# Performance work log

Measured on AMD Instinct MI355X. Metric: run time of the kernel, lower is better.

## Reference

```python
import jax, jax.numpy as jnp
import numpy as np

BS, SEQ, DIM, HEADS = 2, 2048, 1024, 16
HEAD_DIM = DIM // HEADS
NEG = -1e9


def setup_inputs() -> dict:
    key = jax.random.key(0)
    ks = jax.random.split(key, 5)
    s = 1.0 / np.sqrt(DIM)
    return {
        "x": jax.random.normal(ks[0], (BS, SEQ, DIM), jnp.float32),
        "padding_mask": jnp.ones((BS, SEQ), jnp.int32),
        "causal_mask": jnp.tril(jnp.ones((SEQ, SEQ), jnp.int32)),
        "Wq": jax.random.normal(ks[1], (DIM, DIM), jnp.float32) * s,
        "bq": jnp.zeros((DIM,), jnp.float32),
        "Wk": jax.random.normal(ks[2], (DIM, DIM), jnp.float32) * s,
        "bk": jnp.zeros((DIM,), jnp.float32),
        "Wv": jax.random.normal(ks[3], (DIM, DIM), jnp.float32) * s,
        "bv": jnp.zeros((DIM,), jnp.float32),
        "Wo": jax.random.normal(ks[4], (DIM, DIM), jnp.float32) * s,
        "bo": jnp.zeros((DIM,), jnp.float32),
    }


def reference(x, padding_mask, causal_mask, Wq, bq, Wk, bk, Wv, bv, Wo, bo):
    bs, seq, dim = x.shape
    # QKV projections -> [b, h, s, d]
    def proj(W, b):
        return (x @ W.T + b).reshape(bs, seq, HEADS, HEAD_DIM).transpose(0, 2, 1, 3)
    q, k, v = proj(Wq, bq), proj(Wk, bk), proj(Wv, bv)
    scores = jnp.einsum("bhqd,bhkd->bhqk", q, k) / np.sqrt(HEAD_DIM).astype(np.float32)
    scores = jnp.where(padding_mask[:, None, None, :] == 0, NEG, scores)
    scores = jnp.where(causal_mask[None, None, :, :] == 0, NEG, scores)
    attn = jax.nn.softmax(scores, axis=-1)
    out = jnp.einsum("bhqk,bhkd->bhqd", attn, v)
    out = out.transpose(0, 2, 1, 3).reshape(bs, seq, dim)
    return out @ Wo.T + bo
```

## Files before the change

### kernel.cpp

```cpp
#include <hip/hip_runtime.h>
#include <hip/hip_bf16.h>
#include <stdint.h>

#define SEQ 2048
#define DIM 1024
#define HEADS 16
#define HD 64
#define NEGV (-1e9f)
#define SCALE2 0.18033688011112042f
#define THR2 11.541560327111707f

typedef __attribute__((ext_vector_type(8))) short short8;
typedef __attribute__((ext_vector_type(4))) float f32x4;

__device__ __forceinline__ unsigned short f2bf(float f) {
  __hip_bfloat16 h = __float2bfloat16(f);
  union { __hip_bfloat16 h; unsigned short u; } cv;
  cv.h = h;
  return cv.u;
}

__device__ __forceinline__ void async16(const void* g, void* l) {
  __builtin_amdgcn_global_load_lds(
      (const __attribute__((address_space(1))) unsigned int*)g,
      (__attribute__((address_space(3))) unsigned int*)l, 16, 0, 0);
}

__global__ void cast_all_k(const float* __restrict__ x,
                           const float* __restrict__ w0, const float* __restrict__ w1,
                           const float* __restrict__ w2, const float* __restrict__ w3,
                           unsigned short* __restrict__ xo,
                           unsigned short* __restrict__ o0, unsigned short* __restrict__ o1,
                           unsigned short* __restrict__ o2, unsigned short* __restrict__ o3,
                           int nx4, int nw4) {
  const int seg = blockIdx.y;
  const float* in = (seg == 0) ? x : (seg == 1) ? w0 : (seg == 2) ? w1
                   : (seg == 3) ? w2 : w3;
  unsigned short* out = (seg == 0) ? xo : (seg == 1) ? o0 : (seg == 2) ? o1
                       : (seg == 3) ? o2 : o3;
  const int n4 = (seg == 0) ? nx4 : nw4;
  int stride = gridDim.x * blockDim.x;
  for (int i = blockIdx.x * blockDim.x + threadIdx.x; i < n4; i += stride) {
    float4 v = ((const float4*)in)[i];
    ushort4 o;
    o.x = f2bf(v.x); o.y = f2bf(v.y); o.z = f2bf(v.z); o.w = f2bf(v.w);
    ((ushort4*)out)[i] = o;
  }
}

__device__ __forceinline__ void stage_ab(const unsigned short* __restrict__ A,
                                         const unsigned short* __restrict__ B,
                                         int K, int bm0, int bn0, int k0,
                                         unsigned short* As, unsigned short* Bs,
                                         int tid) {
#pragma unroll
  for (int i = 0; i < 2; ++i) {
    int e   = (i * 256 + tid) * 8;
    int row = e >> 5;
    int kk  = e & 31;
    async16(A + (size_t)(bm0 + row) * K + (size_t)(k0 + kk), As + e);
    async16(B + (size_t)(bn0 + row) * K + (size_t)(k0 + kk), Bs + e);
  }
}

__device__ __forceinline__ void gemm_core(const unsigned short* __restrict__ A,
                                          const unsigned short* __restrict__ B,
                                          int K, int bm0, int bn0,
                                          unsigned short (*As)[128 * 32],
                                          unsigned short (*Bs)[128 * 32],
                                          f32x4 acc[4][4]) {
  const int tid  = threadIdx.x;
  const int lane = tid & 63;
  const int w    = tid >> 6;
  const int wr   = w >> 1, wc = w & 1;
  const int lrow = lane & 15, lkg = lane >> 4;

  stage_ab(A, B, K, bm0, bn0, 0, As[0], Bs[0], tid);
  __syncthreads();

  for (int k0 = 0; k0 < K; k0 += 32) {
    const int cur = (k0 >> 5) & 1;
    if (k0 + 32 < K)
      stage_ab(A, B, K, bm0, bn0, k0 + 32, As[cur ^ 1], Bs[cur ^ 1], tid);

    short8 af[4], bf[4];
#pragma unroll
    for (int i = 0; i < 4; ++i) {
      af[i] = *(const short8*)(As[cur] + (wr * 64 + i * 16 + lrow) * 32 + lkg * 8);
      bf[i] = *(const short8*)(Bs[cur] + (wc * 64 + i * 16 + lrow) * 32 + lkg * 8);
    }
#pragma unroll
    for (int i = 0; i < 4; ++i)
#pragma unroll
      for (int j = 0; j < 4; ++j)
        acc[i][j] = __builtin_amdgcn_mfma_f32_16x16x32_bf16(af[i], bf[j], acc[i][j], 0, 0, 0);

    __syncthreads();
  }
}

__global__ __launch_bounds__(256)
void qkv_gemm_k(const unsigned short* __restrict__ xb,
                const unsigned short* __restrict__ wqb,
                const unsigned short* __restrict__ wkb,
                const unsigned short* __restrict__ wvb,
                const float* __restrict__ bq, const float* __restrict__ bk,
                const float* __restrict__ bv,
                unsigned short* __restrict__ Qb, unsigned short* __restrict__ Kb,
                unsigned short* __restrict__ Vtb) {
  __shared__ __align__(16) unsigned short As[2][128 * 32];
  __shared__ __align__(16) unsigned short Bs[2][128 * 32];
  const int z = blockIdx.z;
  const unsigned short* B = (z == 0) ? wqb : (z == 1) ? wkb : wvb;
  const float* bias       = (z == 0) ? bq  : (z == 1) ? bk  : bv;
  const int bm0 = blockIdx.y * 128, bn0 = blockIdx.x * 128;

  f32x4 acc[4][4] = {};
  gemm_core(xb, B, DIM, bm0, bn0, As, Bs, acc);

  const int lane = threadIdx.x & 63;
  const int w = threadIdx.x >> 6, wr = w >> 1, wc = w & 1;
  unsigned short* out01 = (z == 0) ? Qb : Kb;
  const float oscale = (z == 0) ? SCALE2 : 1.0f;
#pragma unroll
  for (int i = 0; i < 4; ++i)
#pragma unroll
    for (int j = 0; j < 4; ++j)
#pragma unroll
      for (int r = 0; r < 4; ++r) {
        int mg = bm0 + wr * 64 + i * 16 + (lane >> 4) * 4 + r;
        int ng = bn0 + wc * 64 + j * 16 + (lane & 15);
        float v = (acc[i][j][r] + bias[ng]) * oscale;
        int bb = mg >> 11, s = mg & 2047, h = ng >> 6, d = ng & 63;
        int bh = bb * HEADS + h;
        if (z < 2)
          out01[((size_t)bh * SEQ + s) * HD + d] = f2bf(v);
        else
          Vtb[((size_t)bh * HD + d) * SEQ + s] = f2bf(v);
      }
}

__global__ __launch_bounds__(256)
void out_gemm_k(const unsigned short* __restrict__ Ob,
                const unsigned short* __restrict__ wob,
                const float* __restrict__ bo, float* __restrict__ out) {
  __shared__ __align__(16) unsigned short As[2][128 * 32];
  __shared__ __align__(16) unsigned short Bs[2][128 * 32];
  const int bm0 = blockIdx.y * 128, bn0 = blockIdx.x * 128;

  f32x4 acc[4][4] = {};
  gemm_core(Ob, wob, DIM, bm0, bn0, As, Bs, acc);

  const int lane = threadIdx.x & 63;
  const int w = threadIdx.x >> 6, wr = w >> 1, wc = w & 1;
#pragma unroll
  for (int i = 0; i < 4; ++i)
#pragma unroll
    for (int j = 0; j < 4; ++j)
#pragma unroll
      for (int r = 0; r < 4; ++r) {
        int mg = bm0 + wr * 64 + i * 16 + (lane >> 4) * 4 + r;
        int ng = bn0 + wc * 64 + j * 16 + (lane & 15);
        out[(size_t)mg * DIM + ng] = acc[i][j][r] + bo[ng];
      }
}

__device__ __forceinline__ void stage_kv64(const unsigned short* __restrict__ kbase,
                                           const unsigned short* __restrict__ vbase,
                                           int k0, unsigned short* KsB,
                                           unsigned short* VsB, int tid) {
#pragma unroll
  for (int j = 0; j < 2; ++j) {
    const int c    = j * 256 + tid;
    const int row  = c >> 3;
    const int colb = (c & 7) << 4;
    const int srcb = colb ^ ((row & 7) << 4);
    async16(kbase + (size_t)(k0 + row) * HD + (srcb >> 1), KsB + c * 8);
  }
#pragma unroll
  for (int j = 0; j < 2; ++j) {
    const int c    = j * 256 + tid;
    const int d    = c >> 3;
    const int colb = (c & 7) << 4;
    const int srcb = colb ^ ((d & 7) << 4);
    async16(vbase + (size_t)d * SEQ + k0 + (srcb >> 1), VsB + c * 8);
  }
}

__global__ __launch_bounds__(256)
void attn_k(const unsigned short* __restrict__ Q,
            const unsigned short* __restrict__ Kp,
            const unsigned short* __restrict__ Vt,
            const int* __restrict__ pm,
            unsigned short* __restrict__ O) {
  __shared__ __align__(16) unsigned short Ks[2][64 * 64];
  __shared__ __align__(16) unsigned short Vs[2][64 * 64];
  __shared__ __align__(16) unsigned short plds[4][16 * 64];

  const int tid  = threadIdx.x;
  const int lane = tid & 63;
  const int w    = tid >> 6;
  const int lc = lane & 15, lg = lane >> 4;
  const int qb = 31 - blockIdx.y;
  const int bh = blockIdx.x;
  const int b  = bh >> 4, h = bh & 15;

  const size_t base = (size_t)bh * SEQ * HD;
  const unsigned short* kbase = Kp + base;
  const unsigned short* vbase = Vt + (size_t)bh * HD * SEQ;
  const int* pmb = pm + b * SEQ;
  char* pb = (char*)&plds[w][0];
  const int swp = (lc & 7) << 4;

  const int qrow0 = qb * 64 + w * 16;
  const int qrow  = qrow0 + lc;

  short8 qa[2];
  {
    const unsigned short* qp = Q + base + (size_t)qrow * HD + lg * 8;
    qa[0] = *(const short8*)(qp);
    qa[1] = *(const short8*)(qp + 32);
  }

  f32x4 oacc[4] = {};
  float mrow = -1e30f, lsum = 0.f;

  const int nk = qb + 1;

  stage_kv64(kbase, vbase, 0, Ks[0], Vs[0], tid);

  int ok = 1;
  for (int i = lane; i < SEQ / 4; i += 64) {
    int4 v = ((const int4*)pmb)[i];
    ok &= (v.x != 0) & (v.y != 0) & (v.z != 0) & (v.w != 0);
  }
  const bool allones = __all(ok);
  __syncthreads();

  for (int kt = 0; kt < nk; ++kt) {
    const int cur = kt & 1;
    const int k0 = kt * 64;
    if (kt + 1 < nk)
      stage_kv64(kbase, vbase, k0 + 64, Ks[cur ^ 1], Vs[cur ^ 1], tid);

    f32x4 s[4];
    const char* kbuf = (const char*)Ks[cur];
    __builtin_amdgcn_s_setprio(1);
#pragma unroll
    for (int t = 0; t < 4; ++t) {
      const int row = t * 16 + lc;
      const int swk = (row & 7) << 4;
      const char* kr = kbuf + row * 128;
      short8 kb0 = *(const short8*)(kr + ((lg * 16) ^ swk));
      short8 kb1 = *(const short8*)(kr + ((lg * 16 + 64) ^ swk));
      f32x4 z = {};
      z = __builtin_amdgcn_mfma_f32_16x16x32_bf16(kb0, qa[0], z, 0, 0, 0);
      z = __builtin_amdgcn_mfma_f32_16x16x32_bf16(kb1, qa[1], z, 0, 0, 0);
      s[t] = z;
    }
    __builtin_amdgcn_s_setprio(0);

    if (!allones) {
#pragma unroll
      for (int t = 0; t < 4; ++t) {
        const int kr0 = k0 + t * 16;
        int4 pmv = *(const int4*)(pmb + kr0 + lg * 4);
#pragma unroll
        for (int r = 0; r < 4; ++r) {
          const int kidx = kr0 + lg * 4 + r;
          if (kidx > qrow || (&pmv.x)[r] == 0) s[t][r] = NEGV;
        }
      }
    } else if (kt == qb) {
#pragma unroll
      for (int t = 0; t < 4; ++t)
#pragma unroll
        for (int r = 0; r < 4; ++r) {
          const int kidx = k0 + t * 16 + lg * 4 + r;
          if (kidx > qrow) s[t][r] = NEGV;
        }
    }

    float mx = -1e30f;
#pragma unroll
    for (int t = 0; t < 4; ++t)
      mx = fmaxf(mx, fmaxf(fmaxf(s[t][0], s[t][1]), fmaxf(s[t][2], s[t][3])));
    if (!__all(mx <= mrow + THR2)) {
      mx = fmaxf(mx, __shfl_xor(mx, 16, 64));
      mx = fmaxf(mx, __shfl_xor(mx, 32, 64));
      const float mnew = fmaxf(mrow, mx);
      const float sc = exp2f(mrow - mnew);
      lsum *= sc;
      mrow = mnew;
      const float s0 = __shfl(sc, lg * 4 + 0, 64);
      const float s1 = __shfl(sc, lg * 4 + 1, 64);
      const float s2 = __shfl(sc, lg * 4 + 2, 64);
      const float s3 = __shfl(sc, lg * 4 + 3, 64);
#pragma unroll
      for (int t = 0; t < 4; ++t) {
        oacc[t][0] *= s0; oacc[t][1] *= s1; oacc[t][2] *= s2; oacc[t][3] *= s3;
      }
    }
    float ps[4];
#pragma unroll
    for (int t = 0; t < 4; ++t) {
      const float p0 = exp2f(s[t][0] - mrow);
      const float p1 = exp2f(s[t][1] - mrow);
      const float p2 = exp2f(s[t][2] - mrow);
      const float p3 = exp2f(s[t][3] - mrow);
      s[t][0] = p0; s[t][1] = p1; s[t][2] = p2; s[t][3] = p3;
      ps[t] = (p0 + p1) + (p2 + p3);
    }
    lsum += (ps[0] + ps[1]) + (ps[2] + ps[3]);

#pragma unroll
    for (int t = 0; t < 4; ++t) {
      short4 pk;
      pk.x = (short)f2bf(s[t][0]); pk.y = (short)f2bf(s[t][1]);
      pk.z = (short)f2bf(s[t][2]); pk.w = (short)f2bf(s[t][3]);
      const int colb = (t * 16 + lg * 4) * 2;
      *(short4*)(pb + lc * 128 + (colb ^ swp)) = pk;
    }
    short8 pa[2];
#pragma unroll
    for (int ks = 0; ks < 2; ++ks)
      pa[ks] = *(const short8*)(pb + lc * 128 + (((ks * 32 + lg * 8) * 2) ^ swp));

    const char* vbuf = (const char*)Vs[cur];
    __builtin_amdgcn_s_setprio(1);
#pragma unroll
    for (int t = 0; t < 4; ++t) {
      const int d = t * 16 + lc;
      const int swv = (d & 7) << 4;
      const char* vr = vbuf + d * 128;
#pragma unroll
      for (int ks = 0; ks < 2; ++ks) {
        short8 vv = *(const short8*)(vr + ((ks * 64 + lg * 16) ^ swv));
        oacc[t] = __builtin_amdgcn_mfma_f32_16x16x32_bf16(pa[ks], vv, oacc[t], 0, 0, 0);
      }
    }
    __builtin_amdgcn_s_setprio(0);

    __syncthreads();
  }

  lsum += __shfl_xor(lsum, 16, 64);
  lsum += __shfl_xor(lsum, 32, 64);
  const float l0 = __shfl(lsum, lg * 4 + 0, 64);
  const float l1 = __shfl(lsum, lg * 4 + 1, 64);
  const float l2 = __shfl(lsum, lg * 4 + 2, 64);
  const float l3 = __shfl(lsum, lg * 4 + 3, 64);
  const float i0 = 1.f / l0, i1 = 1.f / l1, i2 = 1.f / l2, i3 = 1.f / l3;
#pragma unroll
  for (int t = 0; t < 4; ++t) {
    const size_t o0 = ((size_t)(b * SEQ + qrow0 + lg * 4)) * DIM + h * HD + t * 16 + lc;
    O[o0]           = f2bf(oacc[t][0] * i0);
    O[o0 + DIM]     = f2bf(oacc[t][1] * i1);
    O[o0 + 2 * DIM] = f2bf(oacc[t][2] * i2);
    O[o0 + 3 * DIM] = f2bf(oacc[t][3] * i3);
  }
}

extern "C" void kernel_launch(void* const* d_in, const int* in_sizes, int n_in,
                              void* d_out, int out_size, void* d_ws, size_t ws_size,
                              hipStream_t stream) {
  const float* x  = (const float*)d_in[0];
  const int*   pm = (const int*)d_in[1];
  const float* Wq = (const float*)d_in[3];
  const float* bq = (const float*)d_in[4];
  const float* Wk = (const float*)d_in[5];
  const float* bk = (const float*)d_in[6];
  const float* Wv = (const float*)d_in[7];
  const float* bv = (const float*)d_in[8];
  const float* Wo = (const float*)d_in[9];
  const float* bo = (const float*)d_in[10];

  const size_t NX = (size_t)4096 * 1024;
  const size_t NW = (size_t)1024 * 1024;

  unsigned short* ws  = (unsigned short*)d_ws;
  unsigned short* xb  = ws;
  unsigned short* wqb = xb + NX;
  unsigned short* wkb = wqb + NW;
  unsigned short* wvb = wkb + NW;
  unsigned short* wob = wvb + NW;
  unsigned short* Qb  = wob + NW;
  unsigned short* Kb  = Qb + NX;
  unsigned short* Vtb = Kb + NX;
  unsigned short* Ob  = xb;

  cast_all_k<<<dim3(1024, 5), dim3(256), 0, stream>>>(
      x, Wq, Wk, Wv, Wo, xb, wqb, wkb, wvb, wob,
      (int)(NX / 4), (int)(NW / 4));

  qkv_gemm_k<<<dim3(8, 32, 3), dim3(256), 0, stream>>>(xb, wqb, wkb, wvb,
                                                       bq, bk, bv, Qb, Kb, Vtb);

  attn_k<<<dim3(32, 32), dim3(256), 0, stream>>>(Qb, Kb, Vtb, pm, Ob);

  out_gemm_k<<<dim3(8, 32), dim3(256), 0, stream>>>(Ob, wob, bo, (float*)d_out);
}
```

Before: 120.7 us.

## Switch attention to 32x32x16 MFMA with register-resident P via permlane32 swap

Rewrites the attention kernel to use 32x32x16 bf16 MFMA tiles with two 64-lane waves per block, each owning 32 query rows. The softmax probabilities are packed with v_cvt_pk_bf16_f32 and rearranged across lane halves with v_permlane32_swap, so they no longer round-trip through LDS. Block size drops to 128 threads with a min-occupancy hint. The aim is fewer LDS writes and reads and better MFMA efficiency, at the cost of higher register pressure and fewer waves sharing each staged K/V tile.

```diff
diff --git a/kernel.cpp b/kernel.cpp
--- a/kernel.cpp
+++ b/kernel.cpp
@@ -12,6 +12,7 @@
 
 typedef __attribute__((ext_vector_type(8))) short short8;
 typedef __attribute__((ext_vector_type(4))) float f32x4;
+typedef __attribute__((ext_vector_type(16))) float f32x16;
 
 __device__ __forceinline__ unsigned short f2bf(float f) {
   __hip_bfloat16 h = __float2bfloat16(f);
@@ -165,21 +166,21 @@
       }
 }
 
-__device__ __forceinline__ void stage_kv64(const unsigned short* __restrict__ kbase,
-                                           const unsigned short* __restrict__ vbase,
-                                           int k0, unsigned short* KsB,
-                                           unsigned short* VsB, int tid) {
-#pragma unroll
-  for (int j = 0; j < 2; ++j) {
-    const int c    = j * 256 + tid;
+__device__ __forceinline__ void stage_kv64_128(const unsigned short* __restrict__ kbase,
+                                               const unsigned short* __restrict__ vbase,
+                                               int k0, unsigned short* KsB,
+                                               unsigned short* VsB, int tid) {
+#pragma unroll
+  for (int j = 0; j < 4; ++j) {
+    const int c    = j * 128 + tid;
     const int row  = c >> 3;
     const int colb = (c & 7) << 4;
     const int srcb = colb ^ ((row & 7) << 4);
     async16(kbase + (size_t)(k0 + row) * HD + (srcb >> 1), KsB + c * 8);
   }
 #pragma unroll
-  for (int j = 0; j < 2; ++j) {
-    const int c    = j * 256 + tid;
+  for (int j = 0; j < 4; ++j) {
+    const int c    = j * 128 + tid;
     const int d    = c >> 3;
     const int colb = (c & 7) << 4;
     const int srcb = colb ^ ((d & 7) << 4);
@@ -187,7 +188,7 @@
   }
 }
 
-__global__ __launch_bounds__(256)
+__global__ __launch_bounds__(128, 4)
 void attn_k(const unsigned short* __restrict__ Q,
             const unsigned short* __restrict__ Kp,
             const unsigned short* __restrict__ Vt,
@@ -195,12 +196,11 @@
             unsigned short* __restrict__ O) {
   __shared__ __align__(16) unsigned short Ks[2][64 * 64];
   __shared__ __align__(16) unsigned short Vs[2][64 * 64];
-  __shared__ __align__(16) unsigned short plds[4][16 * 64];
 
   const int tid  = threadIdx.x;
   const int lane = tid & 63;
   const int w    = tid >> 6;
-  const int lc = lane & 15, lg = lane >> 4;
+  const int l31 = lane & 31, hi = lane >> 5;
   const int qb = 31 - blockIdx.y;
   const int bh = blockIdx.x;
   const int b  = bh >> 4, h = bh & 15;
@@ -209,25 +209,24 @@
   const unsigned short* kbase = Kp + base;
   const unsigned short* vbase = Vt + (size_t)bh * HD * SEQ;
   const int* pmb = pm + b * SEQ;
-  char* pb = (char*)&plds[w][0];
-  const int swp = (lc & 7) << 4;
-
-  const int qrow0 = qb * 64 + w * 16;
-  const int qrow  = qrow0 + lc;
-
-  short8 qa[2];
+
+  const int qrow0 = qb * 64 + w * 32;
+  const int qrow  = qrow0 + l31;
+
+  short8 qa[4];
   {
-    const unsigned short* qp = Q + base + (size_t)qrow * HD + lg * 8;
-    qa[0] = *(const short8*)(qp);
-    qa[1] = *(const short8*)(qp + 32);
-  }
-
-  f32x4 oacc[4] = {};
+    const unsigned short* qp = Q + base + (size_t)qrow * HD + hi * 8;
+#pragma unroll
+    for (int s = 0; s < 4; ++s) qa[s] = *(const short8*)(qp + s * 16);
+  }
+
+  f32x16 oacc[2] = {};
   float mrow = -1e30f, lsum = 0.f;
 
   const int nk = qb + 1;
-
-  stage_kv64(kbase, vbase, 0, Ks[0], Vs[0], tid);
+  const int swk = (l31 & 7) << 4;
+
+  stage_kv64_128(kbase, vbase, 0, Ks[0], Vs[0], tid);
 
   int ok = 1;
   for (int i = lane; i < SEQ / 4; i += 64) {
@@ -241,123 +240,126 @@
     const int cur = kt & 1;
     const int k0 = kt * 64;
     if (kt + 1 < nk)
-      stage_kv64(kbase, vbase, k0 + 64, Ks[cur ^ 1], Vs[cur ^ 1], tid);
-
-    f32x4 s[4];
+      stage_kv64_128(kbase, vbase, k0 + 64, Ks[cur ^ 1], Vs[cur ^ 1], tid);
+
+    f32x16 z[2];
     const char* kbuf = (const char*)Ks[cur];
     __builtin_amdgcn_s_setprio(1);
 #pragma unroll
-    for (int t = 0; t < 4; ++t) {
-      const int row = t * 16 + lc;
-      const int swk = (row & 7) << 4;
-      const char* kr = kbuf + row * 128;
-      short8 kb0 = *(const short8*)(kr + ((lg * 16) ^ swk));
-      short8 kb1 = *(const short8*)(kr + ((lg * 16 + 64) ^ swk));
-      f32x4 z = {};
-      z = __builtin_amdgcn_mfma_f32_16x16x32_bf16(kb0, qa[0], z, 0, 0, 0);
-      z = __builtin_amdgcn_mfma_f32_16x16x32_bf16(kb1, qa[1], z, 0, 0, 0);
-      s[t] = z;
+    for (int st = 0; st < 2; ++st) {
+      const char* kr = kbuf + (st * 32 + l31) * 128;
+      f32x16 zz = {};
+#pragma unroll
+      for (int s = 0; s < 4; ++s) {
+        short8 ka = *(const short8*)(kr + ((s * 32 + hi * 16) ^ swk));
+        zz = __builtin_amdgcn_mfma_f32_32x32x16_bf16(ka, qa[s], zz, 0, 0, 0);
+      }
+      z[st] = zz;
     }
     __builtin_amdgcn_s_setprio(0);
 
     if (!allones) {
 #pragma unroll
-      for (int t = 0; t < 4; ++t) {
-        const int kr0 = k0 + t * 16;
-        int4 pmv = *(const int4*)(pmb + kr0 + lg * 4);
-#pragma unroll
-        for (int r = 0; r < 4; ++r) {
-          const int kidx = kr0 + lg * 4 + r;
-          if (kidx > qrow || (&pmv.x)[r] == 0) s[t][r] = NEGV;
+      for (int st = 0; st < 2; ++st)
+#pragma unroll
+        for (int r = 0; r < 16; ++r) {
+          const int kidx = k0 + st * 32 + (r & 3) + 8 * (r >> 2) + 4 * hi;
+          if (kidx > qrow || pmb[kidx] == 0) z[st][r] = NEGV;
         }
-      }
     } else if (kt == qb) {
 #pragma unroll
-      for (int t = 0; t < 4; ++t)
-#pragma unroll
-        for (int r = 0; r < 4; ++r) {
-          const int kidx = k0 + t * 16 + lg * 4 + r;
-          if (kidx > qrow) s[t][r] = NEGV;
+      for (int st = 0; st < 2; ++st)
+#pragma unroll
+        for (int r = 0; r < 16; ++r) {
+          const int kidx = k0 + st * 32 + (r & 3) + 8 * (r >> 2) + 4 * hi;
+          if (kidx > qrow) z[st][r] = NEGV;
         }
     }
 
-    float mx = -1e30f;
-#pragma unroll
-    for (int t = 0; t < 4; ++t)
-      mx = fmaxf(mx, fmaxf(fmaxf(s[t][0], s[t][1]), fmaxf(s[t][2], s[t][3])));
+    float m4a = -1e30f, m4b = -1e30f, m4c = -1e30f, m4d = -1e30f;
+#pragma unroll
+    for (int st = 0; st < 2; ++st)
+#pragma unroll
+      for (int r = 0; r < 16; r += 4) {
+        m4a = fmaxf(m4a, z[st][r]);
+        m4b = fmaxf(m4b, z[st][r + 1]);
+        m4c = fmaxf(m4c, z[st][r + 2]);
+        m4d = fmaxf(m4d, z[st][r + 3]);
+      }
+    float mx = fmaxf(fmaxf(m4a, m4b), fmaxf(m4c, m4d));
     if (!__all(mx <= mrow + THR2)) {
-      mx = fmaxf(mx, __shfl_xor(mx, 16, 64));
       mx = fmaxf(mx, __shfl_xor(mx, 32, 64));
       const float mnew = fmaxf(mrow, mx);
       const float sc = exp2f(mrow - mnew);
       lsum *= sc;
       mrow = mnew;
-      const float s0 = __shfl(sc, lg * 4 + 0, 64);
-      const float s1 = __shfl(sc, lg * 4 + 1, 64);
-      const float s2 = __shfl(sc, lg * 4 + 2, 64);
-      const float s3 = __shfl(sc, lg * 4 + 3, 64);
-#pragma unroll
-      for (int t = 0; t < 4; ++t) {
-        oacc[t][0] *= s0; oacc[t][1] *= s1; oacc[t][2] *= s2; oacc[t][3] *= s3;
-      }
-    }
-    float ps[4];
-#pragma unroll
-    for (int t = 0; t < 4; ++t) {
-      const float p0 = exp2f(s[t][0] - mrow);
-      const float p1 = exp2f(s[t][1] - mrow);
-      const float p2 = exp2f(s[t][2] - mrow);
-      const float p3 = exp2f(s[t][3] - mrow);
-      s[t][0] = p0; s[t][1] = p1; s[t][2] = p2; s[t][3] = p3;
-      ps[t] = (p0 + p1) + (p2 + p3);
-    }
-    lsum += (ps[0] + ps[1]) + (ps[2] + ps[3]);
-
-#pragma unroll
-    for (int t = 0; t < 4; ++t) {
-      short4 pk;
-      pk.x = (short)f2bf(s[t][0]); pk.y = (short)f2bf(s[t][1]);
-      pk.z = (short)f2bf(s[t][2]); pk.w = (short)f2bf(s[t][3]);
-      const int colb = (t * 16 + lg * 4) * 2;
-      *(short4*)(pb + lc * 128 + (colb ^ swp)) = pk;
-    }
-    short8 pa[2];
-#pragma unroll
-    for (int ks = 0; ks < 2; ++ks)
-      pa[ks] = *(const short8*)(pb + lc * 128 + (((ks * 32 + lg * 8) * 2) ^ swp));
+      float sct[16];
+#pragma unroll
+      for (int r = 0; r < 16; ++r)
+        sct[r] = __shfl(sc, (r & 3) + 8 * (r >> 2) + 4 * hi, 64);
+#pragma unroll
+      for (int r = 0; r < 16; ++r) {
+        oacc[0][r] *= sct[r];
+        oacc[1][r] *= sct[r];
+      }
+    }
+
+    short8 pa[2][2];
+    float ps = 0.f;
+#pragma unroll
+    for (int st = 0; st < 2; ++st) {
+      float p[16];
+#pragma unroll
+      for (int r = 0; r < 16; ++r) p[r] = exp2f(z[st][r] - mrow);
+      ps += (((p[0] + p[1]) + (p[2] + p[3])) + ((p[4] + p[5]) + (p[6] + p[7]))) +
+            (((p[8] + p[9]) + (p[10] + p[11])) + ((p[12] + p[13]) + (p[14] + p[15])));
+#pragma unroll
+      for (int ks = 0; ks < 2; ++ks) {
+        const int o = ks * 8;
+        unsigned int c0, c1, c2, c3;
+        asm("v_cvt_pk_bf16_f32 %0, %1, %2" : "=v"(c0) : "v"(p[o + 0]), "v"(p[o + 1]));
+        asm("v_cvt_pk_bf16_f32 %0, %1, %2" : "=v"(c1) : "v"(p[o + 2]), "v"(p[o + 3]));
+        asm("v_cvt_pk_bf16_f32 %0, %1, %2" : "=v"(c2) : "v"(p[o + 4]), "v"(p[o + 5]));
+        asm("v_cvt_pk_bf16_f32 %0, %1, %2" : "=v"(c3) : "v"(p[o + 6]), "v"(p[o + 7]));
+        asm volatile("v_permlane32_swap_b32 %0, %1" : "+v"(c0), "+v"(c2));
+        asm volatile("v_permlane32_swap_b32 %0, %1" : "+v"(c1), "+v"(c3));
+        union { unsigned int u[4]; short8 s8; } fr;
+        fr.u[0] = c0; fr.u[1] = c1; fr.u[2] = c2; fr.u[3] = c3;
+        pa[st][ks] = fr.s8;
+      }
+    }
+    lsum += ps;
 
     const char* vbuf = (const char*)Vs[cur];
     __builtin_amdgcn_s_setprio(1);
 #pragma unroll
-    for (int t = 0; t < 4; ++t) {
-      const int d = t * 16 + lc;
-      const int swv = (d & 7) << 4;
-      const char* vr = vbuf + d * 128;
-#pragma unroll
-      for (int ks = 0; ks < 2; ++ks) {
-        short8 vv = *(const short8*)(vr + ((ks * 64 + lg * 16) ^ swv));
-        oacc[t] = __builtin_amdgcn_mfma_f32_16x16x32_bf16(pa[ks], vv, oacc[t], 0, 0, 0);
-      }
+    for (int dt = 0; dt < 2; ++dt) {
+      const char* vr = vbuf + (dt * 32 + l31) * 128;
+#pragma unroll
+      for (int st = 0; st < 2; ++st)
+#pragma unroll
+        for (int ks = 0; ks < 2; ++ks) {
+          short8 vv = *(const short8*)(vr + ((st * 64 + ks * 32 + hi * 16) ^ swk));
+          oacc[dt] = __builtin_amdgcn_mfma_f32_32x32x16_bf16(pa[st][ks], vv,
+                                                             oacc[dt], 0, 0, 0);
+        }
     }
     __builtin_amdgcn_s_setprio(0);
 
     __syncthreads();
   }
 
-  lsum += __shfl_xor(lsum, 16, 64);
   lsum += __shfl_xor(lsum, 32, 64);
-  const float l0 = __shfl(lsum, lg * 4 + 0, 64);
-  const float l1 = __shfl(lsum, lg * 4 + 1, 64);
-  const float l2 = __shfl(lsum, lg * 4 + 2, 64);
-  const float l3 = __shfl(lsum, lg * 4 + 3, 64);
-  const float i0 = 1.f / l0, i1 = 1.f / l1, i2 = 1.f / l2, i3 = 1.f / l3;
-#pragma unroll
-  for (int t = 0; t < 4; ++t) {
-    const size_t o0 = ((size_t)(b * SEQ + qrow0 + lg * 4)) * DIM + h * HD + t * 16 + lc;
-    O[o0]           = f2bf(oacc[t][0] * i0);
-    O[o0 + DIM]     = f2bf(oacc[t][1] * i1);
-    O[o0 + 2 * DIM] = f2bf(oacc[t][2] * i2);
-    O[o0 + 3 * DIM] = f2bf(oacc[t][3] * i3);
+  float il[16];
+#pragma unroll
+  for (int r = 0; r < 16; ++r)
+    il[r] = 1.f / __shfl(lsum, (r & 3) + 8 * (r >> 2) + 4 * hi, 64);
+#pragma unroll
+  for (int r = 0; r < 16; ++r) {
+    const int q_r = (r & 3) + 8 * (r >> 2) + 4 * hi;
+    const size_t o0 = ((size_t)(b * SEQ + qrow0 + q_r)) * DIM + h * HD + l31;
+    O[o0]      = f2bf(oacc[0][r] * il[r]);
+    O[o0 + 32] = f2bf(oacc[1][r] * il[r]);
   }
 }
 
@@ -396,7 +398,7 @@
   qkv_gemm_k<<<dim3(8, 32, 3), dim3(256), 0, stream>>>(xb, wqb, wkb, wvb,
                                                        bq, bk, bv, Qb, Kb, Vtb);
 
-  attn_k<<<dim3(32, 32), dim3(256), 0, stream>>>(Qb, Kb, Vtb, pm, Ob);
+  attn_k<<<dim3(32, 32), dim3(128), 0, stream>>>(Qb, Kb, Vtb, pm, Ob);
 
   out_gemm_k<<<dim3(8, 32), dim3(256), 0, stream>>>(Ob, wob, bo, (float*)d_out);
 }
```

New measurement: 137.4 us. 1.14x slower.
